# Performance work log

Measured on AMD Instinct MI355X. Metric: run time of the kernel, lower is better.

## Reference

```python
import jax, jax.numpy as jnp
import numpy as np


def _sum_of_sqrtm_factors(R1, R2):
    # QR of stacked square-root factors: returns upper-triangular R such that
    # R^T R = R1^T R1 + R2^T R2  (probdiffeq sqrtm.sum_of_sqrtm_factors)
    stacked = jnp.concatenate([R1, R2], axis=0)  # [2n, n]
    return jnp.linalg.qr(stacked, mode='reduced')[1]


def setup_inputs() -> dict:
    key = jax.random.key(0)
    k0, k1, k2, k3, k4 = jax.random.split(key, 5)
    n, d, T = 6, 1024, 4096  # n = num_derivatives + 1
    init_mean = jax.random.normal(k0, (n, d), dtype=jnp.float32)
    init_cov = jax.random.normal(k1, (n, n), dtype=jnp.float32) * 0.1
    # scale transitions so the T-step recursion stays numerically stable
    transitions = jax.random.normal(k2, (T, n, n), dtype=jnp.float32) * 0.2
    noise_means = jax.random.normal(k3, (T, n, d), dtype=jnp.float32)
    noise_covs = jax.random.normal(k4, (T, n, n), dtype=jnp.float32) * 0.1
    return {
        'init_mean': init_mean,
        'init_cov': init_cov,
        'transitions': transitions,
        'noise_means': noise_means,
        'noise_covs': noise_covs,
    }


def reference(init_mean, init_cov, transitions, noise_means, noise_covs):
    """IsotropicImplementation.marginalise_backwards: sequential Kalman
    smoother marginalisation via lax.scan of marginalise_model_isotropic."""

    def body(carry, x):
        m, l = carry                     # m: [n, d], l: [n, n]
        A, n_mean, n_l = x               # A: [n, n], n_mean: [n, d], n_l: [n, n]
        m_new = jnp.dot(A, m) + n_mean
        l_new = _sum_of_sqrtm_factors(jnp.dot(A, l).T, n_l.T).T
        out = (m_new, l_new)
        return out, out

    _, (means, covs) = jax.lax.scan(
        body, (init_mean, init_cov), (transitions, noise_means, noise_covs)
    )
    return means, covs  # [T, n, d], [T, n, n]
```

## Files before the change

kernel.cpp:

```cpp
#include <hip/hip_runtime.h>
#include <stdint.h>

#define T_STEPS 4096
#define DDIM    1024
#define CH      64
#define CL      64
#define MEAN_ELEMS ((size_t)T_STEPS * 6 * DDIM)

#define PF1 8
#define PF3 4

__device__ __forceinline__ float bf2f(uint16_t h){
    return __uint_as_float(((uint32_t)h) << 16);
}
__device__ __forceinline__ uint16_t f2bf(float f){
    uint32_t u = __float_as_uint(f);
    uint32_t r = 0x7FFFu + ((u >> 16) & 1u);
    return (uint16_t)((u + r) >> 16);
}
__device__ __forceinline__ float ld(const void* p, size_t idx, bool f32){
    return f32 ? ((const float*)p)[idx] : bf2f(((const uint16_t*)p)[idx]);
}
template<bool F32>
__device__ __forceinline__ float ldn(const void* p, size_t idx){
    return F32 ? ((const float*)p)[idx] : bf2f(((const uint16_t*)p)[idx]);
}

__device__ __forceinline__ uint32_t detect_wave(const void* imean){
    const uint32_t* w = (const uint32_t*)imean;
    int good = 0;
    for (int i = (int)(threadIdx.x & 63); i < 3072; i += 64){
        float v = bf2f((uint16_t)(w[i] & 0xFFFFu));
        float a = fabsf(v);
        if (a > 1e-6f && a < 1e4f) good++;
    }
    #pragma unroll
    for (int ofs = 32; ofs >= 1; ofs >>= 1) good += __shfl_xor(good, ofs, 64);
    return (good < 2000) ? 1u : 0u;
}

template<bool F32>
__device__ __forceinline__ void km1_body(const void* __restrict__ nmean,
                                         const float* __restrict__ As,
                                         float* __restrict__ r_ws, int c, int col){
    float r[6];
    #pragma unroll
    for (int i = 0; i < 6; ++i) r[i] = 0.f;
    float pb[PF1][6];
    const size_t base = (size_t)c*CL*6144 + col;
    #pragma unroll
    for (int p = 0; p < PF1; ++p)
        #pragma unroll
        for (int i = 0; i < 6; ++i)
            pb[p][i] = ldn<F32>(nmean, base + (size_t)p*6144 + i*DDIM);
    for (int s0 = 0; s0 < CL; s0 += PF1){
        const bool pf = (s0 + PF1 < CL);
        #pragma unroll
        for (int p = 0; p < PF1; ++p){
            const int s = s0 + p;
            float n[6];
            #pragma unroll
            for (int i = 0; i < 6; ++i) n[i] = pb[p][i];
            if (pf){
                #pragma unroll
                for (int i = 0; i < 6; ++i)
                    pb[p][i] = ldn<F32>(nmean, base + (size_t)(s + PF1)*6144 + i*DDIM);
            }
            const float* A = As + s*36;
            float acc[6];
            #pragma unroll
            for (int i = 0; i < 6; ++i){
                float t = n[i];
                #pragma unroll
                for (int m = 0; m < 6; ++m) t += A[i*6+m]*r[m];
                acc[i] = t;
            }
            #pragma unroll
            for (int i = 0; i < 6; ++i) r[i] = acc[i];
        }
    }
    float* out = r_ws + (size_t)c*6144;
    #pragma unroll
    for (int i = 0; i < 6; ++i) out[i*DDIM + col] = r[i];
}

template<bool F32>
__device__ __forceinline__ void km3_body(const void* __restrict__ nmean,
                                         const float* __restrict__ As,
                                         const float* __restrict__ mb_ws,
                                         void* __restrict__ means_out,
                                         int c, int col){
    float m[6];
    const float* mb = mb_ws + (size_t)c*6144;
    #pragma unroll
    for (int i = 0; i < 6; ++i) m[i] = mb[i*DDIM + col];
    float pb[PF3][6];
    const size_t base = (size_t)c*CL*6144 + col;
    #pragma unroll
    for (int p = 0; p < PF3; ++p)
        #pragma unroll
        for (int i = 0; i < 6; ++i)
            pb[p][i] = ldn<F32>(nmean, base + (size_t)p*6144 + i*DDIM);
    for (int s0 = 0; s0 < CL; s0 += PF3){
        const bool pf = (s0 + PF3 < CL);
        #pragma unroll
        for (int p = 0; p < PF3; ++p){
            const int s = s0 + p;
            float n[6];
            #pragma unroll
            for (int i = 0; i < 6; ++i) n[i] = pb[p][i];
            if (pf){
                #pragma unroll
                for (int i = 0; i < 6; ++i)
                    pb[p][i] = ldn<F32>(nmean, base + (size_t)(s + PF3)*6144 + i*DDIM);
            }
            const int k = c*CL + s;
            const float* A = As + s*36;
            float acc[6];
            #pragma unroll
            for (int i = 0; i < 6; ++i){
                float t = n[i];
                #pragma unroll
                for (int mm = 0; mm < 6; ++mm) t += A[i*6+mm]*m[mm];
                acc[i] = t;
            }
            #pragma unroll
            for (int i = 0; i < 6; ++i){
                m[i] = acc[i];
                if (F32){
                    ((float*)means_out)[(size_t)k*6144 + i*DDIM + col] = m[i];
                } else {
                    ((uint16_t*)means_out)[(size_t)k*6144 + i*DDIM + col] = f2bf(m[i]);
                }
            }
        }
    }
}

__global__ void __launch_bounds__(320)
L1_km1_compose(const void* __restrict__ imean, const void* __restrict__ trans,
               const void* __restrict__ ncov, const void* __restrict__ nmean,
               double* __restrict__ Pd, double* __restrict__ Qd,
               float* __restrict__ Pf, float* __restrict__ r_ws){
    __shared__ float As[CL*36], Ns[CL*36];
    __shared__ uint32_t s_flag;
    const int b = blockIdx.x;
    const int c = b >> 2;
    const int tid = threadIdx.x;
    if (tid < 64){
        uint32_t fl = detect_wave(imean);
        if (tid == 0) s_flag = fl;
    }
    __syncthreads();
    const bool f32 = s_flag != 0;
    for (int idx = tid; idx < CL*36; idx += 320){
        const size_t g = (size_t)c*CL*36 + idx;
        As[idx] = ld(trans, g, f32);
        Ns[idx] = ld(ncov,  g, f32);
    }
    __syncthreads();
    if (tid < 256){
        const int col = (b & 3)*256 + tid;
        if (f32) km1_body<true >(nmean, As, r_ws, c, col);
        else     km1_body<false>(nmean, As, r_ws, c, col);
    } else if ((b & 3) == 0){
        const int e  = tid - 256;
        const int ec = (e < 36) ? e : 0;
        const int i = ec / 6, j = ec % 6;
        const int i6 = i*6, j6 = j*6;
        double P = (i == j) ? 1.0 : 0.0, Q = 0.0;
        for (int s = 0; s < CL; ++s){
            const float* A  = As + s*36;
            const float* Nn = Ns + s*36;
            double newP = 0.0, Tij = 0.0;
            #pragma unroll
            for (int m = 0; m < 6; ++m){
                double am = (double)A[i6+m];
                newP += am * __shfl(P, m*6+j, 64);
                Tij  += am * __shfl(Q, m*6+j, 64);
            }
            double qn = 0.0;
            #pragma unroll
            for (int m = 0; m < 6; ++m){
                qn += __shfl(Tij, i6+m, 64) * (double)A[j6+m];
                qn += (double)Nn[i6+m] * (double)Nn[j6+m];
            }
            P = newP; Q = qn;
        }
        if (e < 36){
            Pd[c*36+e] = P;
            Qd[c*36+e] = Q;
            Pf[c*36+e] = (float)P;
        }
    }
}

__global__ void __launch_bounds__(256)
L2_scans(const void* __restrict__ imean, const void* __restrict__ icov,
         const float* __restrict__ Pf,
         const double* __restrict__ Pd, const double* __restrict__ Qd,
         const float* __restrict__ r_ws,
         float* __restrict__ mb_ws, double* __restrict__ Mb){
    __shared__ float  Psf[CH*36];
    __shared__ double Psd[CH*36], Qsd[CH*36], l_ds[36];
    __shared__ uint32_t s_flag;
    const int b = blockIdx.x;
    const int tid = threadIdx.x;
    if (tid < 64){
        uint32_t fl = detect_wave(imean);
        if (tid == 0) s_flag = fl;
    }
    __syncthreads();
    const bool f32 = s_flag != 0;

    if (b < 4){
        for (int idx = tid; idx < CH*36; idx += 256) Psf[idx] = Pf[idx];
        __syncthreads();
        const int col = b*256 + tid;
        float m[6];
        #pragma unroll
        for (int i = 0; i < 6; ++i) m[i] = ld(imean, (size_t)i*DDIM + col, f32);
        float rb[4][6];
        #pragma unroll
        for (int p = 0; p < 4; ++p)
            #pragma unroll
            for (int i = 0; i < 6; ++i) rb[p][i] = r_ws[(size_t)p*6144 + i*DDIM + col];
        for (int c0 = 0; c0 < CH; c0 += 4){
            const bool pf = (c0 + 4 < CH);
            #pragma unroll
            for (int p = 0; p < 4; ++p){
                const int c = c0 + p;
                float rc[6];
                #pragma unroll
                for (int i = 0; i < 6; ++i) rc[i] = rb[p][i];
                if (pf){
                    #pragma unroll
                    for (int i = 0; i < 6; ++i)
                        rb[p][i] = r_ws[(size_t)(c+4)*6144 + i*DDIM + col];
                }
                float* mb = mb_ws + (size_t)c*6144;
                #pragma unroll
                for (int i = 0; i < 6; ++i) mb[i*DDIM + col] = m[i];
                float nm[6];
                #pragma unroll
                for (int i = 0; i < 6; ++i){
                    float s0 = rc[i];
                    #pragma unroll
                    for (int mm = 0; mm < 6; ++mm) s0 += Psf[c*36 + i*6+mm]*m[mm];
                    nm[i] = s0;
                }
                #pragma unroll
                for (int i = 0; i < 6; ++i) m[i] = nm[i];
            }
        }
    } else {
        for (int idx = tid; idx < CH*36; idx += 256){
            Psd[idx] = Pd[idx];
            Qsd[idx] = Qd[idx];
        }
        if (tid < 36) l_ds[tid] = (double)ld(icov, tid, f32);
        __syncthreads();
        if (tid < 64){
            const int e  = tid;
            const int ec = (e < 36) ? e : 0;
            const int i = ec / 6, j = ec % 6;
            const int i6 = i*6, j6 = j*6;
            double M = 0.0;
            #pragma unroll
            for (int mm = 0; mm < 6; ++mm) M += l_ds[i6+mm] * l_ds[j6+mm];
            if (e < 36) Mb[e] = M;
            for (int cc = 0; cc < CH - 1; ++cc){
                const double* Pc = Psd + cc*36;
                double t = 0.0;
                #pragma unroll
                for (int m = 0; m < 6; ++m) t += Pc[i6+m] * __shfl(M, m*6+j, 64);
                double mn = 0.0;
                #pragma unroll
                for (int m = 0; m < 6; ++m) mn += __shfl(t, i6+m, 64) * Pc[j6+m];
                mn += Qsd[cc*36 + ec];
                M = mn;
                if (e < 36) Mb[(cc+1)*36 + e] = mn;
            }
        }
    }
}

__global__ void __launch_bounds__(256)
L3_final(const void* __restrict__ imean, const void* __restrict__ icov,
         const void* __restrict__ trans, const void* __restrict__ ncov,
         const void* __restrict__ nmean,
         const double* __restrict__ Mb, const float* __restrict__ mb_ws,
         void* __restrict__ d_out,
         uint32_t* __restrict__ masks, uint32_t* __restrict__ chunkTot){
    __shared__ float As[CL*36], Ns[CL*36];
    __shared__ double Mst[CL*37];
    __shared__ uint32_t s_flag;
    const int b = blockIdx.x;
    const int tid = threadIdx.x;
    if (tid < 64){
        uint32_t fl = detect_wave(imean);
        if (tid == 0) s_flag = fl;
    }
    __syncthreads();
    const bool f32 = s_flag != 0;

    if (b < 256){
        const int c = b >> 2;
        for (int idx = tid; idx < CL*36; idx += 256)
            As[idx] = ld(trans, (size_t)c*CL*36 + idx, f32);
        __syncthreads();
        const int col = (b & 3)*256 + tid;
        if (f32) km3_body<true >(nmean, As, mb_ws, d_out, c, col);
        else     km3_body<false>(nmean, As, mb_ws, d_out, c, col);
        return;
    }

    const int c = b - 256;
    for (int idx = tid; idx < CL*36; idx += 256){
        const size_t g = (size_t)c*CL*36 + idx;
        As[idx] = ld(trans, g, f32);
        Ns[idx] = ld(ncov,  g, f32);
    }
    __syncthreads();

    if (tid < 64){
        const int e  = tid;
        const int ec = (e < 36) ? e : 0;
        const int i = ec / 6, j = ec % 6;
        const int i6 = i*6, j6 = j*6;
        double M = Mb[c*36 + ec];
        for (int s = 0; ; ++s){
            if (e < 36) Mst[s*37 + e] = M;
            if (s == CL - 1) break;
            const float* A  = As + s*36;
            const float* Nn = Ns + s*36;
            double t = 0.0;
            #pragma unroll
            for (int m = 0; m < 6; ++m) t += (double)A[i6+m] * __shfl(M, m*6+j, 64);
            double mn = 0.0;
            #pragma unroll
            for (int m = 0; m < 6; ++m){
                mn += __shfl(t, i6+m, 64) * (double)A[j6+m];
                mn += (double)Nn[i6+m] * (double)Nn[j6+m];
            }
            M = mn;
        }
    }
    __syncthreads();

    if (tid >= 64) return;
    const int e = tid;
    const int k = c*CL + e;
    double X[12][6];
    if (k == 0){
        double l0[6][6], A0[6][6];
        #pragma unroll
        for (int a = 0; a < 36; ++a){
            l0[a/6][a%6] = (double)ld(icov, a, f32);
            A0[a/6][a%6] = (double)As[a];
        }
        #pragma unroll
        for (int i2 = 0; i2 < 6; ++i2)
            #pragma unroll
            for (int j2 = 0; j2 < 6; ++j2){
                double s = 0.0;
                #pragma unroll
                for (int m = 0; m < 6; ++m) s += A0[i2][m] * l0[m][j2];
                X[j2][i2] = s;
            }
    } else {
        double Mx[6][6];
        #pragma unroll
        for (int a = 0; a < 36; ++a) Mx[a/6][a%6] = Mst[e*37 + a];
        #pragma unroll
        for (int j2 = 0; j2 < 6; ++j2){
            double d = Mx[j2][j2];
            #pragma unroll
            for (int m = 0; m < 6; ++m) if (m < j2) d -= Mx[j2][m]*Mx[j2][m];
            d = (d > 1e-300) ? d : 1e-300;
            double cjj = sqrt(d);
            Mx[j2][j2] = cjj;
            double inv = 1.0 / cjj;
            #pragma unroll
            for (int i2 = 0; i2 < 6; ++i2){
                if (i2 > j2){
                    double s = Mx[i2][j2];
                    #pragma unroll
                    for (int m = 0; m < 6; ++m) if (m < j2) s -= Mx[i2][m]*Mx[j2][m];
                    Mx[i2][j2] = s * inv;
                }
            }
        }
        #pragma unroll
        for (int i2 = 0; i2 < 6; ++i2){
            double Arow[6];
            #pragma unroll
            for (int m = 0; m < 6; ++m) Arow[m] = (double)As[e*36 + i2*6 + m];
            #pragma unroll
            for (int j2 = 0; j2 < 6; ++j2){
                double s = 0.0;
                #pragma unroll
                for (int m = 0; m < 6; ++m) if (m >= j2) s += Arow[m] * Mx[m][j2];
                X[j2][i2] = s;
            }
        }
    }
    #pragma unroll
    for (int r = 0; r < 6; ++r)
        #pragma unroll
        for (int c2 = 0; c2 < 6; ++c2)
            X[6+r][c2] = (double)Ns[e*36 + c2*6 + r];

    #pragma unroll
    for (int kk = 0; kk < 6; ++kk){
        double alpha = X[kk][kk];
        double xn2 = 0.0;
        #pragma unroll
        for (int i2 = 0; i2 < 12; ++i2) if (i2 > kk) xn2 += X[i2][kk]*X[i2][kk];
        if (xn2 != 0.0){
            double nrm  = sqrt(alpha*alpha + xn2);
            double beta = (alpha >= 0.0) ? -nrm : nrm;
            double tau  = (beta - alpha) / beta;
            double sc   = 1.0 / (alpha - beta);
            #pragma unroll
            for (int i2 = 0; i2 < 12; ++i2) if (i2 > kk) X[i2][kk] *= sc;
            X[kk][kk] = beta;
            #pragma unroll
            for (int j2 = 0; j2 < 6; ++j2){
                if (j2 > kk){
                    double w = X[kk][j2];
                    #pragma unroll
                    for (int i2 = 0; i2 < 12; ++i2) if (i2 > kk) w += X[i2][kk]*X[i2][j2];
                    double wt = tau * w;
                    X[kk][j2] -= wt;
                    #pragma unroll
                    for (int i2 = 0; i2 < 12; ++i2) if (i2 > kk) X[i2][j2] -= X[i2][kk]*wt;
                }
            }
        }
    }

    uint32_t mask = 0;
    #pragma unroll
    for (int j2 = 0; j2 < 6; ++j2) if (X[j2][j2] < 0.0) mask |= (1u << j2);
    masks[k] = mask;

    uint32_t incl = mask;
    #pragma unroll
    for (int ofs = 1; ofs < 64; ofs <<= 1){
        uint32_t up = (uint32_t)__shfl_up((int)incl, ofs, 64);
        if (e >= ofs) incl ^= up;
    }
    if (e == 63) chunkTot[c] = incl;

    if (f32){
        float* o = (float*)d_out + MEAN_ELEMS + (size_t)k*36;
        #pragma unroll
        for (int i2 = 0; i2 < 6; ++i2)
            #pragma unroll
            for (int j2 = 0; j2 < 6; ++j2)
                o[i2*6 + j2] = (j2 <= i2) ? (float)X[j2][i2] : 0.0f;
    } else {
        uint16_t* o = (uint16_t*)d_out + MEAN_ELEMS + (size_t)k*36;
        #pragma unroll
        for (int i2 = 0; i2 < 6; ++i2)
            #pragma unroll
            for (int j2 = 0; j2 < 6; ++j2)
                o[i2*6 + j2] = f2bf((j2 <= i2) ? (float)X[j2][i2] : 0.0f);
    }
}

__global__ void __launch_bounds__(64)
L4_sign_apply(const void* __restrict__ imean,
              void* __restrict__ d_out,
              const uint32_t* __restrict__ masks,
              const uint32_t* __restrict__ chunkTot){
    __shared__ uint32_t s_flag;
    const int c = blockIdx.x;
    const int e = threadIdx.x;
    {
        uint32_t fl = detect_wave(imean);
        if (e == 0) s_flag = fl;
    }
    __syncthreads();
    const bool f32 = s_flag != 0;
    const int k = c*CL + e;
    const uint32_t m = masks[k];
    uint32_t incl = m;
    #pragma unroll
    for (int ofs = 1; ofs < 64; ofs <<= 1){
        uint32_t up = (uint32_t)__shfl_up((int)incl, ofs, 64);
        if (e >= ofs) incl ^= up;
    }
    const uint32_t excl = incl ^ m;
    uint32_t v = (e < c) ? chunkTot[e] : 0u;
    #pragma unroll
    for (int ofs = 32; ofs >= 1; ofs >>= 1) v ^= (uint32_t)__shfl_xor((int)v, ofs, 64);
    const uint32_t am = v ^ excl;
    if (am == 0u) return;
    if (f32){
        uint32_t* o = (uint32_t*)d_out + MEAN_ELEMS + (size_t)k*36;
        #pragma unroll
        for (int t = 0; t < 36; ++t)
            if ((am >> (t % 6)) & 1u) o[t] ^= 0x80000000u;
    } else {
        uint16_t* o = (uint16_t*)d_out + MEAN_ELEMS + (size_t)k*36;
        #pragma unroll
        for (int t = 0; t < 36; ++t)
            if ((am >> (t % 6)) & 1u) o[t] ^= 0x8000u;
    }
}

extern "C" void kernel_launch(void* const* d_in, const int* in_sizes, int n_in,
                              void* d_out, int out_size, void* d_ws, size_t ws_size,
                              hipStream_t stream){
    (void)in_sizes; (void)n_in; (void)out_size; (void)ws_size;
    const void* imean = d_in[0];
    const void* icov  = d_in[1];
    const void* trans = d_in[2];
    const void* nmean = d_in[3];
    const void* ncov  = d_in[4];

    char* w = (char*)d_ws;
    double* Pd   = (double*)w; w += (size_t)CH*36*8;
    double* Qd   = (double*)w; w += (size_t)CH*36*8;
    double* Mb   = (double*)w; w += (size_t)CH*36*8;
    float*  Pf   = (float*)w;  w += (size_t)CH*36*4;
    uint32_t* masks    = (uint32_t*)w; w += (size_t)T_STEPS*4;
    uint32_t* chunkTot = (uint32_t*)w; w += (size_t)CH*4;
    float* r_ws  = (float*)w;  w += (size_t)CH*6*DDIM*4;
    float* mb_ws = (float*)w;  w += (size_t)CH*6*DDIM*4;

    L1_km1_compose<<<4*CH, 320, 0, stream>>>(imean, trans, ncov, nmean,
                                             Pd, Qd, Pf, r_ws);
    L2_scans<<<5, 256, 0, stream>>>(imean, icov, Pf, Pd, Qd, r_ws, mb_ws, Mb);
    L3_final<<<4*CH + CH, 256, 0, stream>>>(imean, icov, trans, ncov, nmean,
                                            Mb, mb_ws, d_out, masks, chunkTot);
    L4_sign_apply<<<CH, 64, 0, stream>>>(imean, d_out, masks, chunkTot);
}
```

Before: 366.3 us.

## Split mean-path chunks finer and separate covariance compose blocks

The mean recursion now uses 128 chunks of 32 steps instead of 64 of 64, so twice as many blocks run the parallel per-chunk passes and each block's serial chain is half as long. The covariance composition moves into its own 64 dedicated blocks, which also produce per-half-chunk transition products for the finer mean scan. The r and mb workspaces are merged into one buffer that the L2 scan overwrites in place. In exchange, the sequential L2 scan over chunks doubles in length.

```diff
diff --git a/kernel.cpp b/kernel.cpp
--- a/kernel.cpp
+++ b/kernel.cpp
@@ -5,6 +5,8 @@
 #define DDIM    1024
 #define CH      64
 #define CL      64
+#define MCH     128
+#define MCL     32
 #define MEAN_ELEMS ((size_t)T_STEPS * 6 * DDIM)
 
 #define PF1 8
@@ -47,14 +49,14 @@
     #pragma unroll
     for (int i = 0; i < 6; ++i) r[i] = 0.f;
     float pb[PF1][6];
-    const size_t base = (size_t)c*CL*6144 + col;
+    const size_t base = (size_t)c*MCL*6144 + col;
     #pragma unroll
     for (int p = 0; p < PF1; ++p)
         #pragma unroll
         for (int i = 0; i < 6; ++i)
             pb[p][i] = ldn<F32>(nmean, base + (size_t)p*6144 + i*DDIM);
-    for (int s0 = 0; s0 < CL; s0 += PF1){
-        const bool pf = (s0 + PF1 < CL);
+    for (int s0 = 0; s0 < MCL; s0 += PF1){
+        const bool pf = (s0 + PF1 < MCL);
         #pragma unroll
         for (int p = 0; p < PF1; ++p){
             const int s = s0 + p;
@@ -95,14 +97,14 @@
     #pragma unroll
     for (int i = 0; i < 6; ++i) m[i] = mb[i*DDIM + col];
     float pb[PF3][6];
-    const size_t base = (size_t)c*CL*6144 + col;
+    const size_t base = (size_t)c*MCL*6144 + col;
     #pragma unroll
     for (int p = 0; p < PF3; ++p)
         #pragma unroll
         for (int i = 0; i < 6; ++i)
             pb[p][i] = ldn<F32>(nmean, base + (size_t)p*6144 + i*DDIM);
-    for (int s0 = 0; s0 < CL; s0 += PF3){
-        const bool pf = (s0 + PF3 < CL);
+    for (int s0 = 0; s0 < MCL; s0 += PF3){
+        const bool pf = (s0 + PF3 < MCL);
         #pragma unroll
         for (int p = 0; p < PF3; ++p){
             const int s = s0 + p;
@@ -114,7 +116,7 @@
                 for (int i = 0; i < 6; ++i)
                     pb[p][i] = ldn<F32>(nmean, base + (size_t)(s + PF3)*6144 + i*DDIM);
             }
-            const int k = c*CL + s;
+            const int k = c*MCL + s;
             const float* A = As + s*36;
             float acc[6];
             #pragma unroll
@@ -137,15 +139,14 @@
     }
 }
 
-__global__ void __launch_bounds__(320)
-L1_km1_compose(const void* __restrict__ imean, const void* __restrict__ trans,
+__global__ void __launch_bounds__(256)
+LA_km1_compose(const void* __restrict__ imean, const void* __restrict__ trans,
                const void* __restrict__ ncov, const void* __restrict__ nmean,
                double* __restrict__ Pd, double* __restrict__ Qd,
                float* __restrict__ Pf, float* __restrict__ r_ws){
     __shared__ float As[CL*36], Ns[CL*36];
     __shared__ uint32_t s_flag;
     const int b = blockIdx.x;
-    const int c = b >> 2;
     const int tid = threadIdx.x;
     if (tid < 64){
         uint32_t fl = detect_wave(imean);
@@ -153,45 +154,59 @@
     }
     __syncthreads();
     const bool f32 = s_flag != 0;
-    for (int idx = tid; idx < CL*36; idx += 320){
+
+    if (b < 512){
+        const int mc = b >> 2;
+        for (int idx = tid; idx < MCL*36; idx += 256)
+            As[idx] = ld(trans, (size_t)mc*MCL*36 + idx, f32);
+        __syncthreads();
+        const int col = (b & 3)*256 + tid;
+        if (f32) km1_body<true >(nmean, As, r_ws, mc, col);
+        else     km1_body<false>(nmean, As, r_ws, mc, col);
+        return;
+    }
+
+    const int c = b - 512;
+    for (int idx = tid; idx < CL*36; idx += 256){
         const size_t g = (size_t)c*CL*36 + idx;
         As[idx] = ld(trans, g, f32);
         Ns[idx] = ld(ncov,  g, f32);
     }
     __syncthreads();
-    if (tid < 256){
-        const int col = (b & 3)*256 + tid;
-        if (f32) km1_body<true >(nmean, As, r_ws, c, col);
-        else     km1_body<false>(nmean, As, r_ws, c, col);
-    } else if ((b & 3) == 0){
-        const int e  = tid - 256;
-        const int ec = (e < 36) ? e : 0;
-        const int i = ec / 6, j = ec % 6;
-        const int i6 = i*6, j6 = j*6;
-        double P = (i == j) ? 1.0 : 0.0, Q = 0.0;
-        for (int s = 0; s < CL; ++s){
-            const float* A  = As + s*36;
-            const float* Nn = Ns + s*36;
-            double newP = 0.0, Tij = 0.0;
-            #pragma unroll
-            for (int m = 0; m < 6; ++m){
-                double am = (double)A[i6+m];
-                newP += am * __shfl(P, m*6+j, 64);
-                Tij  += am * __shfl(Q, m*6+j, 64);
-            }
-            double qn = 0.0;
-            #pragma unroll
-            for (int m = 0; m < 6; ++m){
-                qn += __shfl(Tij, i6+m, 64) * (double)A[j6+m];
-                qn += (double)Nn[i6+m] * (double)Nn[j6+m];
-            }
-            P = newP; Q = qn;
-        }
-        if (e < 36){
-            Pd[c*36+e] = P;
-            Qd[c*36+e] = Q;
-            Pf[c*36+e] = (float)P;
-        }
+    if (tid >= 64) return;
+    const int e  = tid;
+    const int ec = (e < 36) ? e : 0;
+    const int i = ec / 6, j = ec % 6;
+    const int i6 = i*6, j6 = j*6;
+    double P = (i == j) ? 1.0 : 0.0, Q = 0.0;
+    double Pm = (i == j) ? 1.0 : 0.0;
+    for (int s = 0; s < CL; ++s){
+        const float* A  = As + s*36;
+        const float* Nn = Ns + s*36;
+        double newP = 0.0, Tij = 0.0, newPm = 0.0;
+        #pragma unroll
+        for (int m = 0; m < 6; ++m){
+            double am = (double)A[i6+m];
+            newP  += am * __shfl(P,  m*6+j, 64);
+            Tij   += am * __shfl(Q,  m*6+j, 64);
+            newPm += am * __shfl(Pm, m*6+j, 64);
+        }
+        double qn = 0.0;
+        #pragma unroll
+        for (int m = 0; m < 6; ++m){
+            qn += __shfl(Tij, i6+m, 64) * (double)A[j6+m];
+            qn += (double)Nn[i6+m] * (double)Nn[j6+m];
+        }
+        P = newP; Q = qn; Pm = newPm;
+        if (s == CL/2 - 1){
+            if (e < 36) Pf[(size_t)(2*c)*36 + e] = (float)Pm;
+            Pm = (i == j) ? 1.0 : 0.0;
+        }
+    }
+    if (e < 36){
+        Pd[c*36+e] = P;
+        Qd[c*36+e] = Q;
+        Pf[(size_t)(2*c+1)*36 + e] = (float)Pm;
     }
 }
 
@@ -199,9 +214,8 @@
 L2_scans(const void* __restrict__ imean, const void* __restrict__ icov,
          const float* __restrict__ Pf,
          const double* __restrict__ Pd, const double* __restrict__ Qd,
-         const float* __restrict__ r_ws,
-         float* __restrict__ mb_ws, double* __restrict__ Mb){
-    __shared__ float  Psf[CH*36];
+         float* __restrict__ rmb_ws, double* __restrict__ Mb){
+    __shared__ float  Psf[MCH*36];
     __shared__ double Psd[CH*36], Qsd[CH*36], l_ds[36];
     __shared__ uint32_t s_flag;
     const int b = blockIdx.x;
@@ -214,7 +228,7 @@
     const bool f32 = s_flag != 0;
 
     if (b < 4){
-        for (int idx = tid; idx < CH*36; idx += 256) Psf[idx] = Pf[idx];
+        for (int idx = tid; idx < MCH*36; idx += 256) Psf[idx] = Pf[idx];
         __syncthreads();
         const int col = b*256 + tid;
         float m[6];
@@ -224,9 +238,9 @@
         #pragma unroll
         for (int p = 0; p < 4; ++p)
             #pragma unroll
-            for (int i = 0; i < 6; ++i) rb[p][i] = r_ws[(size_t)p*6144 + i*DDIM + col];
-        for (int c0 = 0; c0 < CH; c0 += 4){
-            const bool pf = (c0 + 4 < CH);
+            for (int i = 0; i < 6; ++i) rb[p][i] = rmb_ws[(size_t)p*6144 + i*DDIM + col];
+        for (int c0 = 0; c0 < MCH; c0 += 4){
+            const bool pf = (c0 + 4 < MCH);
             #pragma unroll
             for (int p = 0; p < 4; ++p){
                 const int c = c0 + p;
@@ -236,9 +250,9 @@
                 if (pf){
                     #pragma unroll
                     for (int i = 0; i < 6; ++i)
-                        rb[p][i] = r_ws[(size_t)(c+4)*6144 + i*DDIM + col];
+                        rb[p][i] = rmb_ws[(size_t)(c+4)*6144 + i*DDIM + col];
                 }
-                float* mb = mb_ws + (size_t)c*6144;
+                float* mb = rmb_ws + (size_t)c*6144;
                 #pragma unroll
                 for (int i = 0; i < 6; ++i) mb[i*DDIM + col] = m[i];
                 float nm[6];
@@ -289,7 +303,7 @@
 L3_final(const void* __restrict__ imean, const void* __restrict__ icov,
          const void* __restrict__ trans, const void* __restrict__ ncov,
          const void* __restrict__ nmean,
-         const double* __restrict__ Mb, const float* __restrict__ mb_ws,
+         const double* __restrict__ Mb, const float* __restrict__ rmb_ws,
          void* __restrict__ d_out,
          uint32_t* __restrict__ masks, uint32_t* __restrict__ chunkTot){
     __shared__ float As[CL*36], Ns[CL*36];
@@ -304,18 +318,18 @@
     __syncthreads();
     const bool f32 = s_flag != 0;
 
-    if (b < 256){
-        const int c = b >> 2;
-        for (int idx = tid; idx < CL*36; idx += 256)
-            As[idx] = ld(trans, (size_t)c*CL*36 + idx, f32);
+    if (b < 512){
+        const int mc = b >> 2;
+        for (int idx = tid; idx < MCL*36; idx += 256)
+            As[idx] = ld(trans, (size_t)mc*MCL*36 + idx, f32);
         __syncthreads();
         const int col = (b & 3)*256 + tid;
-        if (f32) km3_body<true >(nmean, As, mb_ws, d_out, c, col);
-        else     km3_body<false>(nmean, As, mb_ws, d_out, c, col);
+        if (f32) km3_body<true >(nmean, As, rmb_ws, d_out, mc, col);
+        else     km3_body<false>(nmean, As, rmb_ws, d_out, mc, col);
         return;
     }
 
-    const int c = b - 256;
+    const int c = b - 512;
     for (int idx = tid; idx < CL*36; idx += 256){
         const size_t g = (size_t)c*CL*36 + idx;
         As[idx] = ld(trans, g, f32);
@@ -525,16 +539,15 @@
     double* Pd   = (double*)w; w += (size_t)CH*36*8;
     double* Qd   = (double*)w; w += (size_t)CH*36*8;
     double* Mb   = (double*)w; w += (size_t)CH*36*8;
-    float*  Pf   = (float*)w;  w += (size_t)CH*36*4;
+    float*  Pf   = (float*)w;  w += (size_t)MCH*36*4;
     uint32_t* masks    = (uint32_t*)w; w += (size_t)T_STEPS*4;
     uint32_t* chunkTot = (uint32_t*)w; w += (size_t)CH*4;
-    float* r_ws  = (float*)w;  w += (size_t)CH*6*DDIM*4;
-    float* mb_ws = (float*)w;  w += (size_t)CH*6*DDIM*4;
-
-    L1_km1_compose<<<4*CH, 320, 0, stream>>>(imean, trans, ncov, nmean,
-                                             Pd, Qd, Pf, r_ws);
-    L2_scans<<<5, 256, 0, stream>>>(imean, icov, Pf, Pd, Qd, r_ws, mb_ws, Mb);
-    L3_final<<<4*CH + CH, 256, 0, stream>>>(imean, icov, trans, ncov, nmean,
-                                            Mb, mb_ws, d_out, masks, chunkTot);
+    float* rmb_ws = (float*)w; w += (size_t)MCH*6*DDIM*4;
+
+    LA_km1_compose<<<512 + CH, 256, 0, stream>>>(imean, trans, ncov, nmean,
+                                                 Pd, Qd, Pf, rmb_ws);
+    L2_scans<<<5, 256, 0, stream>>>(imean, icov, Pf, Pd, Qd, rmb_ws, Mb);
+    L3_final<<<512 + CH, 256, 0, stream>>>(imean, icov, trans, ncov, nmean,
+                                           Mb, rmb_ws, d_out, masks, chunkTot);
     L4_sign_apply<<<CH, 64, 0, stream>>>(imean, d_out, masks, chunkTot);
 }
```

Result: faster. 305.7 us (-16.6%).
